# Kernel tuning notes

Measured on AMD Instinct MI355X. Metric: run time of the kernel, lower is better.

Reference implementation:

```python
import jax, jax.numpy as jnp
import numpy as np

INPUT_DIM = 2048
NUM_EXPERTS = 64
TOP_K = 2


def setup_inputs() -> dict:
    key = jax.random.key(0)
    kx, kw = jax.random.split(key)
    x = jax.random.normal(kx, (4, 4096, INPUT_DIM), dtype=jnp.float32)
    # nn.Linear weight has shape [num_experts, input_dim]
    W = jax.random.normal(kw, (NUM_EXPERTS, INPUT_DIM), dtype=jnp.float32) * (INPUT_DIM ** -0.5)
    return {"x": x, "W": W}


def reference(x, W):
    # Flatten tokens: [N, D]
    x_flat = x.reshape(-1, INPUT_DIM)
    # Gate logits: [N, E]
    gate_logits = jnp.einsum("nd,ed->ne", x_flat, W)
    # Top-k (sorted descending, matching torch.topk)
    top_k_logits, top_k_indices = jax.lax.top_k(gate_logits, TOP_K)
    top_k_values = jax.nn.softmax(top_k_logits, axis=-1)
    return (top_k_indices, top_k_values)
```

## Files before the change

### kernel.cpp

```cpp
#include <hip/hip_runtime.h>
#include <hip/hip_bf16.h>
#include <math.h>

typedef float f4 __attribute__((ext_vector_type(4)));
typedef float f32x4 __attribute__((ext_vector_type(4)));
typedef short bf16x8 __attribute__((ext_vector_type(8)));

#define D      2048
#define NE     64
#define TOKB   16
#define KSPLIT 8
#define KRNG   (D / KSPLIT)
#define KCH    32
#define NCH    (KRNG / KCH)
#define LROW   40
#define SLAB   5120
#define CSTR   68

__device__ __forceinline__ unsigned short bf16rne(float f) {
    unsigned int u = __builtin_bit_cast(unsigned int, f);
    u += 0x7fffu + ((u >> 16) & 1u);
    return (unsigned short)(u >> 16);
}
__device__ __forceinline__ float bf2f(unsigned short h) {
    unsigned int u = (unsigned int)h << 16;
    return __builtin_bit_cast(float, u);
}

__global__ __launch_bounds__(256)
void wprep(const float* __restrict__ W,
           unsigned short* __restrict__ Whp,
           unsigned short* __restrict__ Wlp)
{
    const int i  = blockIdx.x * 256 + threadIdx.x;
    const int j  = i & 7;
    const int l  = (i >> 3) & 63;
    const int et = (i >> 9) & 3;
    const int kc = i >> 11;
    const int e  = et * 16 + (l & 15);
    const int k  = kc * 32 + (l >> 4) * 8 + j;
    const float w = W[(size_t)e * D + k];
    const unsigned short h = bf16rne(w);
    Whp[i] = h;
    Wlp[i] = bf16rne(w - bf2f(h));
}

#define CVTPAIR(F0, F1, HOUT, LOUT) {                                        \
    __hip_bfloat162 hp_ = __float22bfloat162_rn(make_float2((F0), (F1)));    \
    unsigned hu_; __builtin_memcpy(&hu_, &hp_, 4);                           \
    const float h0_ = __builtin_bit_cast(float, hu_ << 16);                  \
    const float h1_ = __builtin_bit_cast(float, hu_ & 0xffff0000u);          \
    __hip_bfloat162 lp_ = __float22bfloat162_rn(                             \
        make_float2((F0) - h0_, (F1) - h1_));                                \
    unsigned lu_; __builtin_memcpy(&lu_, &lp_, 4);                           \
    HOUT = hu_;                                                              \
    LOUT = lu_;                                                              \
}

__global__ __launch_bounds__(512, 4)
void moe_fused(const float* __restrict__ x,
               const unsigned short* __restrict__ Whp,
               const unsigned short* __restrict__ Wlp,
               float* __restrict__ out, int ntok)
{
    __shared__ __align__(16) char smem[KSPLIT][SLAB];

    const int t    = threadIdx.x;
    const int w    = t >> 6;
    const int l    = t & 63;
    const int tok0 = blockIdx.x * TOKB;
    const int k0   = w * KRNG;

    unsigned short* stg = (unsigned short*)smem[w];

    const int srow = l >> 3;
    const int sg   = l & 7;
    const int ar   = l & 15;
    const int akb  = (l >> 4) * 8;

    const float* xbase = x + (size_t)tok0 * D + k0 + sg * 4;
    const unsigned short* whp = Whp + (size_t)w * 16384 + l * 8;
    const unsigned short* wlp = Wlp + (size_t)w * 16384 + l * 8;

#define LOADX(ch, R0, R1) { \
    const float* p_ = xbase + (ch) * KCH; \
    R0 = *(const f4*)(p_ + (size_t)(srow    ) * D); \
    R1 = *(const f4*)(p_ + (size_t)(srow + 8) * D); }

#define CVT1(v, buf, row) { \
    uint2 hw_, lw_; \
    CVTPAIR(v.x, v.y, hw_.x, lw_.x); \
    CVTPAIR(v.z, v.w, hw_.y, lw_.y); \
    *(uint2*)&stg[(((buf)*2 + 0)*TOKB + (row))*LROW + sg*4] = hw_; \
    *(uint2*)&stg[(((buf)*2 + 1)*TOKB + (row))*LROW + sg*4] = lw_; }

#define CVTWR(buf, R0, R1) { CVT1(R0, buf, srow); CVT1(R1, buf, srow + 8); }

#define CHUNK(ch, buf) { \
    bf16x8 bh[4], bl[4]; \
    _Pragma("unroll") \
    for (int et = 0; et < 4; ++et) { \
        const size_t o_ = (size_t)(4 * (ch) + et) * 512; \
        bh[et] = *(const bf16x8*)(whp + o_); \
        bl[et] = *(const bf16x8*)(wlp + o_); \
    } \
    const bf16x8 ah = *(const bf16x8*)&stg[(((buf)*2 + 0)*TOKB + ar)*LROW + akb]; \
    const bf16x8 al = *(const bf16x8*)&stg[(((buf)*2 + 1)*TOKB + ar)*LROW + akb]; \
    _Pragma("unroll") \
    for (int et = 0; et < 4; ++et) { \
        acc[et] = __builtin_amdgcn_mfma_f32_16x16x32_bf16(ah, bh[et], acc[et], 0, 0, 0); \
        acc[et] = __builtin_amdgcn_mfma_f32_16x16x32_bf16(ah, bl[et], acc[et], 0, 0, 0); \
        acc[et] = __builtin_amdgcn_mfma_f32_16x16x32_bf16(al, bh[et], acc[et], 0, 0, 0); \
    } }

    const f32x4 zz = {0.f, 0.f, 0.f, 0.f};
    f32x4 acc[4] = {zz, zz, zz, zz};

    f4 xE0, xE1, xO0, xO1;

    LOADX(0, xE0, xE1);
    LOADX(1, xO0, xO1);
    CVTWR(0, xE0, xE1);
    LOADX(2, xE0, xE1);

#pragma unroll
    for (int ch = 0; ch < NCH; ch += 2) {
        CHUNK(ch, 0);
        CVTWR(1, xO0, xO1);
        if (ch + 3 < NCH) LOADX(ch + 3, xO0, xO1);
        CHUNK(ch + 1, 1);
        if (ch + 2 < NCH) CVTWR(0, xE0, xE1);
        if (ch + 4 < NCH) LOADX(ch + 4, xE0, xE1);
    }

#undef LOADX
#undef CVT1
#undef CVTWR
#undef CHUNK

    float* cred = (float*)smem[w];
#pragma unroll
    for (int et = 0; et < 4; ++et)
#pragma unroll
        for (int r = 0; r < 4; ++r) {
            const int tokl = (l >> 4) * 4 + r;
            cred[tokl * CSTR + et * 16 + (l & 15)] = acc[et][r];
        }
    __syncthreads();

    if (t < TOKB * 8) {
        const int tokl = t >> 3;
        const int eg   = t & 7;
        f4 s0 = {0.f,0.f,0.f,0.f}, s1 = {0.f,0.f,0.f,0.f};
#pragma unroll
        for (int ww = 0; ww < KSPLIT; ++ww) {
            const float* cw = (const float*)smem[ww] + tokl * CSTR + eg * 8;
            s0 += *(const f4*)cw;
            s1 += *(const f4*)(cw + 4);
        }
        const float vv[8] = {s0.x, s0.y, s0.z, s0.w, s1.x, s1.y, s1.z, s1.w};
        float m1 = -INFINITY, m2 = -INFINITY;
        int i1 = 0, i2 = 0;
#pragma unroll
        for (int j = 0; j < 8; ++j) {
            const float v = vv[j];
            const int id = eg * 8 + j;
            if (v > m1)      { m2 = m1; i2 = i1; m1 = v; i1 = id; }
            else if (v > m2) { m2 = v;  i2 = id; }
        }
#pragma unroll
        for (int m = 1; m < 8; m <<= 1) {
            const float om1 = __shfl_xor(m1, m);
            const int   oi1 = __shfl_xor(i1, m);
            const float om2 = __shfl_xor(m2, m);
            const int   oi2 = __shfl_xor(i2, m);
            const bool b1 = (om1 > m1) || (om1 == m1 && oi1 < i1);
            const float c2v = b1 ? m1 : om1;  const int c2i = b1 ? i1 : oi1;
            const float c3v = b1 ? om2 : m2;  const int c3i = b1 ? oi2 : i2;
            if (b1) { m1 = om1; i1 = oi1; }
            const bool b2 = (c3v > c2v) || (c3v == c2v && c3i < c2i);
            m2 = b2 ? c3v : c2v;  i2 = b2 ? c3i : c2i;
        }
        if (eg == 0) {
            const int tok = tok0 + tokl;
            out[(size_t)tok * 2 + 0] = (float)i1;
            out[(size_t)tok * 2 + 1] = (float)i2;
            const float p1 = 1.0f / (1.0f + expf(m2 - m1));
            float* vals = out + (size_t)ntok * 2;
            vals[(size_t)tok * 2 + 0] = p1;
            vals[(size_t)tok * 2 + 1] = 1.0f - p1;
        }
    }
}

extern "C" void kernel_launch(void* const* d_in, const int* in_sizes, int n_in,
                              void* d_out, int out_size, void* d_ws, size_t ws_size,
                              hipStream_t stream)
{
    const float* x = (const float*)d_in[0];
    const float* W = (const float*)d_in[1];
    float* out = (float*)d_out;
    unsigned short* Whp = (unsigned short*)d_ws;
    unsigned short* Wlp = Whp + (size_t)NE * D;

    const int ntok = in_sizes[0] / D;
    wprep<<<(NE * D) / 256, 256, 0, stream>>>(W, Whp, Wlp);
    moe_fused<<<ntok / TOKB, 512, 0, stream>>>(x, Whp, Wlp, out, ntok);
}
```

Baseline: 41.68 us.

## Double tokens per block to reuse each W fragment across two row tiles

Raises the tokens per block from 16 to 32. Each wave now loads and converts four x rows per lane and runs MFMAs over two 16-row tiles, using the same bf16 hi/lo W fragments for both. This halves the W global/L2 traffic per token and halves the grid size. In exchange it doubles LDS per block to 80KB and adds accumulator and x-prefetch registers, which may lower occupancy (launch bounds still ask for 4 blocks). The reduction stage now covers 32 tokens with all 256 threads.

Result: no change. 40.93 us (-1.8%).

```diff
diff --git a/kernel.cpp b/kernel.cpp
--- a/kernel.cpp
+++ b/kernel.cpp
@@ -8,13 +8,13 @@
 
 #define D      2048
 #define NE     64
-#define TOKB   16
+#define TOKB   32
 #define KSPLIT 8
 #define KRNG   (D / KSPLIT)
 #define KCH    32
 #define NCH    (KRNG / KCH)
 #define LROW   40
-#define SLAB   5120
+#define SLAB   10240
 #define CSTR   68
 
 __device__ __forceinline__ unsigned short bf16rne(float f) {
@@ -69,7 +69,6 @@
     const int w    = t >> 6;
     const int l    = t & 63;
     const int tok0 = blockIdx.x * TOKB;
-    const int k0   = w * KRNG;
 
     unsigned short* stg = (unsigned short*)smem[w];
 
@@ -78,14 +77,16 @@
     const int ar   = l & 15;
     const int akb  = (l >> 4) * 8;
 
-    const float* xbase = x + (size_t)tok0 * D + k0 + sg * 4;
+    const float* xbase = x + (size_t)tok0 * D + w * KRNG + sg * 4;
     const unsigned short* whp = Whp + (size_t)w * 16384 + l * 8;
     const unsigned short* wlp = Wlp + (size_t)w * 16384 + l * 8;
 
-#define LOADX(ch, R0, R1) { \
+#define LOADX(ch, R0, R1, R2, R3) { \
     const float* p_ = xbase + (ch) * KCH; \
-    R0 = *(const f4*)(p_ + (size_t)(srow    ) * D); \
-    R1 = *(const f4*)(p_ + (size_t)(srow + 8) * D); }
+    R0 = *(const f4*)(p_ + (size_t)(srow     ) * D); \
+    R1 = *(const f4*)(p_ + (size_t)(srow +  8) * D); \
+    R2 = *(const f4*)(p_ + (size_t)(srow + 16) * D); \
+    R3 = *(const f4*)(p_ + (size_t)(srow + 24) * D); }
 
 #define CVT1(v, buf, row) { \
     uint2 hw_, lw_; \
@@ -94,7 +95,9 @@
     *(uint2*)&stg[(((buf)*2 + 0)*TOKB + (row))*LROW + sg*4] = hw_; \
     *(uint2*)&stg[(((buf)*2 + 1)*TOKB + (row))*LROW + sg*4] = lw_; }
 
-#define CVTWR(buf, R0, R1) { CVT1(R0, buf, srow); CVT1(R1, buf, srow + 8); }
+#define CVTWR(buf, R0, R1, R2, R3) { \
+    CVT1(R0, buf, srow);      CVT1(R1, buf, srow + 8); \
+    CVT1(R2, buf, srow + 16); CVT1(R3, buf, srow + 24); }
 
 #define CHUNK(ch, buf) { \
     bf16x8 bh[4], bl[4]; \
@@ -104,33 +107,44 @@
         bh[et] = *(const bf16x8*)(whp + o_); \
         bl[et] = *(const bf16x8*)(wlp + o_); \
     } \
-    const bf16x8 ah = *(const bf16x8*)&stg[(((buf)*2 + 0)*TOKB + ar)*LROW + akb]; \
-    const bf16x8 al = *(const bf16x8*)&stg[(((buf)*2 + 1)*TOKB + ar)*LROW + akb]; \
+    bf16x8 ah[2], al[2]; \
+    _Pragma("unroll") \
+    for (int rt = 0; rt < 2; ++rt) { \
+        const int row_ = rt * 16 + ar; \
+        ah[rt] = *(const bf16x8*)&stg[(((buf)*2 + 0)*TOKB + row_)*LROW + akb]; \
+        al[rt] = *(const bf16x8*)&stg[(((buf)*2 + 1)*TOKB + row_)*LROW + akb]; \
+    } \
+    _Pragma("unroll") \
+    for (int rt = 0; rt < 2; ++rt) \
     _Pragma("unroll") \
     for (int et = 0; et < 4; ++et) { \
-        acc[et] = __builtin_amdgcn_mfma_f32_16x16x32_bf16(ah, bh[et], acc[et], 0, 0, 0); \
-        acc[et] = __builtin_amdgcn_mfma_f32_16x16x32_bf16(ah, bl[et], acc[et], 0, 0, 0); \
-        acc[et] = __builtin_amdgcn_mfma_f32_16x16x32_bf16(al, bh[et], acc[et], 0, 0, 0); \
+        acc[rt][et] = __builtin_amdgcn_mfma_f32_16x16x32_bf16(ah[rt], bh[et], acc[rt][et], 0, 0, 0); \
+        acc[rt][et] = __builtin_amdgcn_mfma_f32_16x16x32_bf16(ah[rt], bl[et], acc[rt][et], 0, 0, 0); \
+        acc[rt][et] = __builtin_amdgcn_mfma_f32_16x16x32_bf16(al[rt], bh[et], acc[rt][et], 0, 0, 0); \
     } }
 
     const f32x4 zz = {0.f, 0.f, 0.f, 0.f};
-    f32x4 acc[4] = {zz, zz, zz, zz};
-
-    f4 xE0, xE1, xO0, xO1;
-
-    LOADX(0, xE0, xE1);
-    LOADX(1, xO0, xO1);
-    CVTWR(0, xE0, xE1);
-    LOADX(2, xE0, xE1);
+    f32x4 acc[2][4];
+#pragma unroll
+    for (int i = 0; i < 2; ++i)
+#pragma unroll
+        for (int j = 0; j < 4; ++j) acc[i][j] = zz;
+
+    f4 xE0, xE1, xE2, xE3, xO0, xO1, xO2, xO3;
+
+    LOADX(0, xE0, xE1, xE2, xE3);
+    LOADX(1, xO0, xO1, xO2, xO3);
+    CVTWR(0, xE0, xE1, xE2, xE3);
+    LOADX(2, xE0, xE1, xE2, xE3);
 
 #pragma unroll
     for (int ch = 0; ch < NCH; ch += 2) {
         CHUNK(ch, 0);
-        CVTWR(1, xO0, xO1);
-        if (ch + 3 < NCH) LOADX(ch + 3, xO0, xO1);
+        CVTWR(1, xO0, xO1, xO2, xO3);
+        if (ch + 3 < NCH) LOADX(ch + 3, xO0, xO1, xO2, xO3);
         CHUNK(ch + 1, 1);
-        if (ch + 2 < NCH) CVTWR(0, xE0, xE1);
-        if (ch + 4 < NCH) LOADX(ch + 4, xE0, xE1);
+        if (ch + 2 < NCH) CVTWR(0, xE0, xE1, xE2, xE3);
+        if (ch + 4 < NCH) LOADX(ch + 4, xE0, xE1, xE2, xE3);
     }
 
 #undef LOADX
@@ -140,12 +154,14 @@
 
     float* cred = (float*)smem[w];
 #pragma unroll
-    for (int et = 0; et < 4; ++et)
-#pragma unroll
-        for (int r = 0; r < 4; ++r) {
-            const int tokl = (l >> 4) * 4 + r;
-            cred[tokl * CSTR + et * 16 + (l & 15)] = acc[et][r];
-        }
+    for (int rt = 0; rt < 2; ++rt)
+#pragma unroll
+        for (int et = 0; et < 4; ++et)
+#pragma unroll
+            for (int r = 0; r < 4; ++r) {
+                const int tokl = rt * 16 + (l >> 4) * 4 + r;
+                cred[tokl * CSTR + et * 16 + (l & 15)] = acc[rt][et][r];
+            }
     __syncthreads();
 
     if (t < TOKB * 8) {
```

## Cut register pressure to double occupancy with shallower x prefetch pipeline

Applied to the files above, without the earlier changes.

Raises the launch-bounds occupancy hint from 4 to 8 blocks per SM-equivalent, and shrinks the x prefetch pipeline from two chunks ahead to one. The weight fragments are now loaded per expert tile inside the MFMA loop instead of all up front. This frees registers so more waves can be resident to hide memory latency. The cost is less in-wave prefetch depth, and weight loads sit closer to their use. LDS per block (40KB) may still cap the number of resident blocks regardless of the hint.

Measured after the change: 44.48 us. 1.07x slower.

```diff
diff --git a/kernel.cpp b/kernel.cpp
--- a/kernel.cpp
+++ b/kernel.cpp
@@ -57,7 +57,7 @@
     LOUT = lu_;                                                              \
 }
 
-__global__ __launch_bounds__(512, 4)
+__global__ __launch_bounds__(512, 8)
 void moe_fused(const float* __restrict__ x,
                const unsigned short* __restrict__ Whp,
                const unsigned short* __restrict__ Wlp,
@@ -69,7 +69,6 @@
     const int w    = t >> 6;
     const int l    = t & 63;
     const int tok0 = blockIdx.x * TOKB;
-    const int k0   = w * KRNG;
 
     unsigned short* stg = (unsigned short*)smem[w];
 
@@ -78,14 +77,14 @@
     const int ar   = l & 15;
     const int akb  = (l >> 4) * 8;
 
-    const float* xbase = x + (size_t)tok0 * D + k0 + sg * 4;
+    const float* xbase = x + (size_t)tok0 * D + w * KRNG + sg * 4;
     const unsigned short* whp = Whp + (size_t)w * 16384 + l * 8;
     const unsigned short* wlp = Wlp + (size_t)w * 16384 + l * 8;
 
-#define LOADX(ch, R0, R1) { \
+#define LOADX(ch) { \
     const float* p_ = xbase + (ch) * KCH; \
-    R0 = *(const f4*)(p_ + (size_t)(srow    ) * D); \
-    R1 = *(const f4*)(p_ + (size_t)(srow + 8) * D); }
+    xr0 = *(const f4*)(p_ + (size_t)(srow    ) * D); \
+    xr1 = *(const f4*)(p_ + (size_t)(srow + 8) * D); }
 
 #define CVT1(v, buf, row) { \
     uint2 hw_, lw_; \
@@ -94,43 +93,34 @@
     *(uint2*)&stg[(((buf)*2 + 0)*TOKB + (row))*LROW + sg*4] = hw_; \
     *(uint2*)&stg[(((buf)*2 + 1)*TOKB + (row))*LROW + sg*4] = lw_; }
 
-#define CVTWR(buf, R0, R1) { CVT1(R0, buf, srow); CVT1(R1, buf, srow + 8); }
+#define CVTWR(buf) { CVT1(xr0, buf, srow); CVT1(xr1, buf, srow + 8); }
 
 #define CHUNK(ch, buf) { \
-    bf16x8 bh[4], bl[4]; \
-    _Pragma("unroll") \
-    for (int et = 0; et < 4; ++et) { \
-        const size_t o_ = (size_t)(4 * (ch) + et) * 512; \
-        bh[et] = *(const bf16x8*)(whp + o_); \
-        bl[et] = *(const bf16x8*)(wlp + o_); \
-    } \
     const bf16x8 ah = *(const bf16x8*)&stg[(((buf)*2 + 0)*TOKB + ar)*LROW + akb]; \
     const bf16x8 al = *(const bf16x8*)&stg[(((buf)*2 + 1)*TOKB + ar)*LROW + akb]; \
     _Pragma("unroll") \
     for (int et = 0; et < 4; ++et) { \
-        acc[et] = __builtin_amdgcn_mfma_f32_16x16x32_bf16(ah, bh[et], acc[et], 0, 0, 0); \
-        acc[et] = __builtin_amdgcn_mfma_f32_16x16x32_bf16(ah, bl[et], acc[et], 0, 0, 0); \
-        acc[et] = __builtin_amdgcn_mfma_f32_16x16x32_bf16(al, bh[et], acc[et], 0, 0, 0); \
+        const size_t o_ = (size_t)(4 * (ch) + et) * 512; \
+        const bf16x8 bh = *(const bf16x8*)(whp + o_); \
+        const bf16x8 bl = *(const bf16x8*)(wlp + o_); \
+        acc[et] = __builtin_amdgcn_mfma_f32_16x16x32_bf16(ah, bh, acc[et], 0, 0, 0); \
+        acc[et] = __builtin_amdgcn_mfma_f32_16x16x32_bf16(ah, bl, acc[et], 0, 0, 0); \
+        acc[et] = __builtin_amdgcn_mfma_f32_16x16x32_bf16(al, bh, acc[et], 0, 0, 0); \
     } }
 
     const f32x4 zz = {0.f, 0.f, 0.f, 0.f};
     f32x4 acc[4] = {zz, zz, zz, zz};
 
-    f4 xE0, xE1, xO0, xO1;
+    f4 xr0, xr1;
 
-    LOADX(0, xE0, xE1);
-    LOADX(1, xO0, xO1);
-    CVTWR(0, xE0, xE1);
-    LOADX(2, xE0, xE1);
+    LOADX(0);
+    CVTWR(0);
 
 #pragma unroll
-    for (int ch = 0; ch < NCH; ch += 2) {
-        CHUNK(ch, 0);
-        CVTWR(1, xO0, xO1);
-        if (ch + 3 < NCH) LOADX(ch + 3, xO0, xO1);
-        CHUNK(ch + 1, 1);
-        if (ch + 2 < NCH) CVTWR(0, xE0, xE1);
-        if (ch + 4 < NCH) LOADX(ch + 4, xE0, xE1);
+    for (int ch = 0; ch < NCH; ++ch) {
+        if (ch + 1 < NCH) LOADX(ch + 1);
+        CHUNK(ch, ch & 1);
+        if (ch + 1 < NCH) CVTWR((ch + 1) & 1);
     }
 
 #undef LOADX
```

## Load x directly in MFMA operand layout and drop LDS staging

Applied to the files above, without the earlier changes.

Each lane now loads the eight consecutive x floats it needs for the MFMA A operand directly from global memory, splits them into bf16 hi/lo in registers, and passes them straight to the MFMA. This removes the LDS staging buffer and its write/read round trip, and shrinks shared memory to just the reduction buffer. The launch-bounds occupancy hint rises from 4 to 6 blocks. The trade-off is less coalesced global loads: each lane reads 32 bytes from a different token row, and the 6-block hint may raise register pressure.

Result: slower. 46.24 us (+10.9%).

```diff
diff --git a/kernel.cpp b/kernel.cpp
--- a/kernel.cpp
+++ b/kernel.cpp
@@ -5,6 +5,7 @@
 typedef float f4 __attribute__((ext_vector_type(4)));
 typedef float f32x4 __attribute__((ext_vector_type(4)));
 typedef short bf16x8 __attribute__((ext_vector_type(8)));
+typedef unsigned int u32x4 __attribute__((ext_vector_type(4)));
 
 #define D      2048
 #define NE     64
@@ -13,8 +14,6 @@
 #define KRNG   (D / KSPLIT)
 #define KCH    32
 #define NCH    (KRNG / KCH)
-#define LROW   40
-#define SLAB   5120
 #define CSTR   68
 
 __device__ __forceinline__ unsigned short bf16rne(float f) {
@@ -57,46 +56,32 @@
     LOUT = lu_;                                                              \
 }
 
-__global__ __launch_bounds__(512, 4)
+__global__ __launch_bounds__(512, 6)
 void moe_fused(const float* __restrict__ x,
                const unsigned short* __restrict__ Whp,
                const unsigned short* __restrict__ Wlp,
                float* __restrict__ out, int ntok)
 {
-    __shared__ __align__(16) char smem[KSPLIT][SLAB];
+    __shared__ float cred[KSPLIT][TOKB * CSTR];
 
     const int t    = threadIdx.x;
     const int w    = t >> 6;
     const int l    = t & 63;
     const int tok0 = blockIdx.x * TOKB;
-    const int k0   = w * KRNG;
 
-    unsigned short* stg = (unsigned short*)smem[w];
+    const int ar  = l & 15;
+    const int akb = (l >> 4) * 8;
 
-    const int srow = l >> 3;
-    const int sg   = l & 7;
-    const int ar   = l & 15;
-    const int akb  = (l >> 4) * 8;
-
-    const float* xbase = x + (size_t)tok0 * D + k0 + sg * 4;
+    const float* xa = x + (size_t)(tok0 + ar) * D + w * KRNG + akb;
     const unsigned short* whp = Whp + (size_t)w * 16384 + l * 8;
     const unsigned short* wlp = Wlp + (size_t)w * 16384 + l * 8;
 
 #define LOADX(ch, R0, R1) { \
-    const float* p_ = xbase + (ch) * KCH; \
-    R0 = *(const f4*)(p_ + (size_t)(srow    ) * D); \
-    R1 = *(const f4*)(p_ + (size_t)(srow + 8) * D); }
+    const float* p_ = xa + (ch) * KCH; \
+    R0 = *(const f4*)(p_);     \
+    R1 = *(const f4*)(p_ + 4); }
 
-#define CVT1(v, buf, row) { \
-    uint2 hw_, lw_; \
-    CVTPAIR(v.x, v.y, hw_.x, lw_.x); \
-    CVTPAIR(v.z, v.w, hw_.y, lw_.y); \
-    *(uint2*)&stg[(((buf)*2 + 0)*TOKB + (row))*LROW + sg*4] = hw_; \
-    *(uint2*)&stg[(((buf)*2 + 1)*TOKB + (row))*LROW + sg*4] = lw_; }
-
-#define CVTWR(buf, R0, R1) { CVT1(R0, buf, srow); CVT1(R1, buf, srow + 8); }
-
-#define CHUNK(ch, buf) { \
+#define CHUNK(ch, R0, R1) { \
     bf16x8 bh[4], bl[4]; \
     _Pragma("unroll") \
     for (int et = 0; et < 4; ++et) { \
@@ -104,8 +89,16 @@
         bh[et] = *(const bf16x8*)(whp + o_); \
         bl[et] = *(const bf16x8*)(wlp + o_); \
     } \
-    const bf16x8 ah = *(const bf16x8*)&stg[(((buf)*2 + 0)*TOKB + ar)*LROW + akb]; \
-    const bf16x8 al = *(const bf16x8*)&stg[(((buf)*2 + 1)*TOKB + ar)*LROW + akb]; \
+    unsigned hu0_, hu1_, hu2_, hu3_, lu0_, lu1_, lu2_, lu3_; \
+    CVTPAIR(R0.x, R0.y, hu0_, lu0_); \
+    CVTPAIR(R0.z, R0.w, hu1_, lu1_); \
+    CVTPAIR(R1.x, R1.y, hu2_, lu2_); \
+    CVTPAIR(R1.z, R1.w, hu3_, lu3_); \
+    const u32x4 hv_ = {hu0_, hu1_, hu2_, hu3_}; \
+    const u32x4 lv_ = {lu0_, lu1_, lu2_, lu3_}; \
+    const bf16x8 ah = __builtin_bit_cast(bf16x8, hv_); \
+    const bf16x8 al = __builtin_bit_cast(bf16x8, lv_); \
+    if ((ch) + 2 < NCH) LOADX((ch) + 2, R0, R1); \
     _Pragma("unroll") \
     for (int et = 0; et < 4; ++et) { \
         acc[et] = __builtin_amdgcn_mfma_f32_16x16x32_bf16(ah, bh[et], acc[et], 0, 0, 0); \
@@ -120,31 +113,22 @@
 
     LOADX(0, xE0, xE1);
     LOADX(1, xO0, xO1);
-    CVTWR(0, xE0, xE1);
-    LOADX(2, xE0, xE1);
 
 #pragma unroll
     for (int ch = 0; ch < NCH; ch += 2) {
-        CHUNK(ch, 0);
-        CVTWR(1, xO0, xO1);
-        if (ch + 3 < NCH) LOADX(ch + 3, xO0, xO1);
-        CHUNK(ch + 1, 1);
-        if (ch + 2 < NCH) CVTWR(0, xE0, xE1);
-        if (ch + 4 < NCH) LOADX(ch + 4, xE0, xE1);
+        CHUNK(ch,     xE0, xE1);
+        CHUNK(ch + 1, xO0, xO1);
     }
 
 #undef LOADX
-#undef CVT1
-#undef CVTWR
 #undef CHUNK
 
-    float* cred = (float*)smem[w];
 #pragma unroll
     for (int et = 0; et < 4; ++et)
 #pragma unroll
         for (int r = 0; r < 4; ++r) {
             const int tokl = (l >> 4) * 4 + r;
-            cred[tokl * CSTR + et * 16 + (l & 15)] = acc[et][r];
+            cred[w][tokl * CSTR + et * 16 + (l & 15)] = acc[et][r];
         }
     __syncthreads();
 
@@ -154,7 +138,7 @@
         f4 s0 = {0.f,0.f,0.f,0.f}, s1 = {0.f,0.f,0.f,0.f};
 #pragma unroll
         for (int ww = 0; ww < KSPLIT; ++ww) {
-            const float* cw = (const float*)smem[ww] + tokl * CSTR + eg * 8;
+            const float* cw = &cred[ww][tokl * CSTR + eg * 8];
             s0 += *(const f4*)cw;
             s1 += *(const f4*)(cw + 4);
         }
```
